# Kernel optimization log

Hardware: AMD Instinct MI355X
Metric: run time of the kernel (lower is better)

Reference implementation:

```python
import jax, jax.numpy as jnp
import numpy as np

T, E, D, F, K, CAP = 4096, 8, 1024, 4096, 2, 1024


def setup_inputs() -> dict:
    key = jax.random.key(0)
    ks = jax.random.split(key, 4)
    x = jax.random.normal(ks[0], (T, D), jnp.float32)
    # top-k routing: mask/weight consistent with a softmax router
    logits = jax.random.normal(ks[1], (T, E), jnp.float32)
    probs = jax.nn.softmax(logits, axis=-1)
    _, topi = jax.lax.top_k(probs, K)  # (T, K)
    route_mask = jnp.zeros((T, E), jnp.bool_).at[jnp.arange(T)[:, None], topi].set(True)
    route_weight = jnp.where(route_mask, probs, 0.0)
    # stacked expert MLP params (E leading axis, as ModuleGroup stacks them)
    w1 = jax.random.normal(ks[2], (E, D, F), jnp.float32) * 0.02
    b1 = jnp.zeros((E, F), jnp.float32)
    w2 = jax.random.normal(ks[3], (E, F, D), jnp.float32) * 0.02
    b2 = jnp.zeros((E, D), jnp.float32)
    return dict(x=x, route_mask=route_mask, route_weight=route_weight,
                w1=w1, b1=b1, w2=w2, b2=b2)


def _build_slots(mask_te, w_te, cap):
    # mask_te: (T,E) bool; w_te: (T,E) float (0 where unrouted)
    Tn, En = mask_te.shape
    m_et = mask_te.T                              # (E,T)
    w_et = jnp.where(m_et, w_te.T, -jnp.inf)      # unrouted -> -inf
    _, idx_top = jax.lax.top_k(w_et, cap)         # (E,C) token ids per slot
    slot = jnp.zeros((En, cap, Tn), w_te.dtype)
    slot = slot.at[jnp.arange(En)[:, None], jnp.arange(cap)[None, :], idx_top].set(1.0)
    slot = slot * m_et[:, None, :].astype(w_te.dtype)  # zero slots from -inf picks
    # NOTE: the original re-orders slots along C (a stable sort); the combine
    # einsum sums over C so the output is invariant to slot order -- skipped.
    return slot


def reference(x, route_mask, route_weight, w1, b1, w2, b2):
    w_te = jnp.where(route_mask, route_weight, 0.0)      # (T,E)
    slot = _build_slots(route_mask, w_te, CAP)           # (E,C,T) one-hot
    # dispatch: 'ect,t...->ec...'
    xs = jnp.einsum('ect,td->ecd', slot, x)              # (E,C,D)
    # expert compute (vmapped MLP over E)
    h = jax.nn.gelu(jnp.einsum('ecd,edf->ecf', xs, w1) + b1[:, None, :])
    out = jnp.einsum('ecf,efd->ecd', h, w2) + b2[:, None, :]
    # combine: 'ecf,ect,te->tf'
    y = jnp.einsum('ecd,ect,te->td', out, slot, w_te)    # (T,D)
    return y
```

## Files before the change

kernel.cpp:

```cpp
#include <hip/hip_runtime.h>
#include <hip/hip_bf16.h>
#include <stdint.h>

#define T_TOK 4096
#define E_EXP 8
#define D_DIM 1024
#define F_DIM 4096
#define K_TOP 2
#define CAPC  1024

typedef __attribute__((ext_vector_type(8))) short short8;
typedef __attribute__((ext_vector_type(4))) float f32x4;
typedef __attribute__((ext_vector_type(4))) unsigned short u16x4;

static __device__ __forceinline__ unsigned short f2bf(float f) {
  union { float f; unsigned u; } v; v.f = f;
  unsigned r = v.u + 0x7fffu + ((v.u >> 16) & 1u);
  return (unsigned short)(r >> 16);
}

static __device__ __forceinline__ void gload_lds16(const void* g, void* l) {
  __builtin_amdgcn_global_load_lds(
      (const __attribute__((address_space(1))) unsigned int*)g,
      (__attribute__((address_space(3))) unsigned int*)l, 16, 0, 0);
}

__global__ void zero_int_kernel(int* p, int n) {
  int i = blockIdx.x * 256 + threadIdx.x;
  if (i < n) p[i] = 0;
}

__global__ __launch_bounds__(1024) void select_kernel(
    const float* __restrict__ rw,
    int* __restrict__ sel_idx,
    int* __restrict__ inv_cnt,
    int* __restrict__ inv_ec,
    float* __restrict__ inv_w)
{
  __shared__ unsigned long long keys[T_TOK];
  const int e = blockIdx.x;
  for (int t = threadIdx.x; t < T_TOK; t += 1024) {
    float w = rw[(size_t)t * E_EXP + e];
    unsigned wb = __float_as_uint(w);
    keys[t] = (w > 0.f)
        ? ((((unsigned long long)wb) << 32) | (unsigned)(T_TOK - 1 - t))
        : 0ull;
  }
  for (int k = 2; k <= T_TOK; k <<= 1) {
    for (int j = k >> 1; j > 0; j >>= 1) {
      __syncthreads();
      for (int i = threadIdx.x; i < T_TOK; i += 1024) {
        int ixj = i ^ j;
        if (ixj > i) {
          unsigned long long a = keys[i], b = keys[ixj];
          bool sw = ((i & k) == 0) ? (a < b) : (a > b);
          if (sw) { keys[i] = b; keys[ixj] = a; }
        }
      }
    }
  }
  __syncthreads();
  for (int c = threadIdx.x; c < CAPC; c += 1024) {
    unsigned long long key = keys[c];
    int t = -1; float w = 0.f;
    if ((key >> 32) != 0ull) {
      t = T_TOK - 1 - (int)(key & 0xffffffffu);
      w = __uint_as_float((unsigned)(key >> 32));
    }
    sel_idx[e * CAPC + c] = t;
    if (t >= 0) {
      int p = atomicAdd(&inv_cnt[t], 1);
      inv_ec[t * K_TOP + p] = e * CAPC + c;
      inv_w[t * K_TOP + p] = w;
    }
  }
}

__global__ void convert_x_kernel(const float* __restrict__ x,
                                 unsigned short* __restrict__ xb, int n4) {
  int i = blockIdx.x * 256 + threadIdx.x;
  if (i >= n4) return;
  f32x4 v = ((const f32x4*)x)[i];
  u16x4 o = { f2bf(v.x), f2bf(v.y), f2bf(v.z), f2bf(v.w) };
  ((u16x4*)xb)[i] = o;
}

__global__ __launch_bounds__(256) void transpose_bf16_kernel(
    const float* __restrict__ in, unsigned short* __restrict__ out,
    int R, int C)
{
  __shared__ unsigned short tile[64][68];
  const int e = blockIdx.z;
  const float* inp = in + (size_t)e * R * C;
  unsigned short* outp = out + (size_t)e * R * C;
  const int c0 = blockIdx.x * 64, r0 = blockIdx.y * 64;
  const int q4 = (threadIdx.x & 15) * 4;
  const int tr = threadIdx.x >> 4;
  for (int rr = tr; rr < 64; rr += 16) {
    f32x4 v = *(const f32x4*)(inp + (size_t)(r0 + rr) * C + c0 + q4);
    tile[rr][q4 + 0] = f2bf(v.x);
    tile[rr][q4 + 1] = f2bf(v.y);
    tile[rr][q4 + 2] = f2bf(v.z);
    tile[rr][q4 + 3] = f2bf(v.w);
  }
  __syncthreads();
  for (int cc = tr; cc < 64; cc += 16) {
    u16x4 o = { tile[q4 + 0][cc], tile[q4 + 1][cc],
                tile[q4 + 2][cc], tile[q4 + 3][cc] };
    *(u16x4*)(outp + (size_t)(c0 + cc) * R + r0 + q4) = o;
  }
}


__global__ __launch_bounds__(256, 3) void gemm1_kernel(
    const unsigned short* __restrict__ xb,
    const int* __restrict__ sel_idx,
    const unsigned short* __restrict__ w1t,
    const float* __restrict__ b1,
    unsigned short* __restrict__ H)
{
  __shared__ __align__(16) unsigned short Asm[128 * 64];
  __shared__ __align__(16) unsigned short Bsm[128 * 64];
  const int e = blockIdx.z;
  const int m0 = blockIdx.y * 128;
  const int n0 = blockIdx.x * 128;
  const int tid = threadIdx.x;
  const int lane = tid & 63, wv = tid >> 6;
  const int wm = (wv >> 1) * 64, wn = (wv & 1) * 64;
  const int lrow = lane & 15, quad = lane >> 4;

  const int rbase = tid >> 3, seg = tid & 7;
  const int cs = seg ^ (rbase & 7);
  const unsigned short* gA[4];
  const unsigned short* gB[4];
  char* lA[4];
  char* lB[4];
  const unsigned short* w1e = w1t + (size_t)e * F_DIM * D_DIM;
#pragma unroll
  for (int it = 0; it < 4; ++it) {
    const int row = rbase + it * 32;
    int t = sel_idx[e * CAPC + m0 + row];
    if (t < 0) t = 0;
    gA[it] = xb + (size_t)t * D_DIM + cs * 8;
    gB[it] = w1e + (size_t)(n0 + row) * D_DIM + cs * 8;
    lA[it] = (char*)Asm + it * 4096 + wv * 1024;
    lB[it] = (char*)Bsm + it * 4096 + wv * 1024;
  }

  f32x4 acc[4][4];
#pragma unroll
  for (int a = 0; a < 4; ++a)
#pragma unroll
    for (int b = 0; b < 4; ++b) acc[a][b] = (f32x4){0.f, 0.f, 0.f, 0.f};

  const int sw = lrow & 7;
  for (int k0 = 0; k0 < D_DIM; k0 += 64) {
#pragma unroll
    for (int it = 0; it < 4; ++it) { gload_lds16(gA[it], lA[it]); gA[it] += 64; }
#pragma unroll
    for (int it = 0; it < 4; ++it) { gload_lds16(gB[it], lB[it]); gB[it] += 64; }
    __syncthreads();
#pragma unroll
    for (int h = 0; h < 2; ++h) {
      short8 af[4], bf[4];
#pragma unroll
      for (int mt = 0; mt < 4; ++mt)
        af[mt] = *(const short8*)(Asm + (wm + mt * 16 + lrow) * 64 +
                                  (((h << 2) + quad) ^ sw) * 8);
#pragma unroll
      for (int nt = 0; nt < 4; ++nt)
        bf[nt] = *(const short8*)(Bsm + (wn + nt * 16 + lrow) * 64 +
                                  (((h << 2) + quad) ^ sw) * 8);
#pragma unroll
      for (int mt = 0; mt < 4; ++mt)
#pragma unroll
        for (int nt = 0; nt < 4; ++nt)
          acc[mt][nt] = __builtin_amdgcn_mfma_f32_16x16x32_bf16(
              af[mt], bf[nt], acc[mt][nt], 0, 0, 0);
    }
    __syncthreads();
  }

  const float* b1e = b1 + e * F_DIM;
#pragma unroll
  for (int nt = 0; nt < 4; ++nt) {
    const int col = n0 + wn + nt * 16 + lrow;
    const float bias = b1e[col];
#pragma unroll
    for (int mt = 0; mt < 4; ++mt) {
      const int rowb = m0 + wm + mt * 16 + quad * 4;
#pragma unroll
      for (int i = 0; i < 4; ++i) {
        float v = acc[mt][nt][i] + bias;
        float u = 0.7978845608028654f * (v + 0.044715f * v * v * v);
        float th = 1.f - 2.f / (1.f + __expf(2.f * u));
        float hv = 0.5f * v * (1.f + th);
        H[((size_t)e * CAPC + rowb + i) * F_DIM + col] = f2bf(hv);
      }
    }
  }
}

__global__ __launch_bounds__(256, 3) void gemm2_kernel(
    const unsigned short* __restrict__ H,
    const unsigned short* __restrict__ w2t,
    const float* __restrict__ b2,
    float* __restrict__ P)
{
  __shared__ __align__(16) unsigned short Asm[128 * 64];
  __shared__ __align__(16) unsigned short Bsm[128 * 64];
  const int e = blockIdx.z & 7;
  const int ks = blockIdx.z >> 3;
  const int m0 = blockIdx.y * 128;
  const int n0 = blockIdx.x * 128;
  const int kbase = ks * (F_DIM / 2);
  const int tid = threadIdx.x;
  const int lane = tid & 63, wv = tid >> 6;
  const int wm = (wv >> 1) * 64, wn = (wv & 1) * 64;
  const int lrow = lane & 15, quad = lane >> 4;

  const int rbase = tid >> 3, seg = tid & 7;
  const int cs = seg ^ (rbase & 7);
  const unsigned short* gA[4];
  const unsigned short* gB[4];
  char* lA[4];
  char* lB[4];
  const unsigned short* He = H + (size_t)e * CAPC * F_DIM;
  const unsigned short* w2e = w2t + (size_t)e * D_DIM * F_DIM;
#pragma unroll
  for (int it = 0; it < 4; ++it) {
    const int row = rbase + it * 32;
    gA[it] = He + (size_t)(m0 + row) * F_DIM + kbase + cs * 8;
    gB[it] = w2e + (size_t)(n0 + row) * F_DIM + kbase + cs * 8;
    lA[it] = (char*)Asm + it * 4096 + wv * 1024;
    lB[it] = (char*)Bsm + it * 4096 + wv * 1024;
  }

  f32x4 acc[4][4];
#pragma unroll
  for (int a = 0; a < 4; ++a)
#pragma unroll
    for (int b = 0; b < 4; ++b) acc[a][b] = (f32x4){0.f, 0.f, 0.f, 0.f};

  const int sw = lrow & 7;
  for (int k0 = 0; k0 < F_DIM / 2; k0 += 64) {
#pragma unroll
    for (int it = 0; it < 4; ++it) { gload_lds16(gA[it], lA[it]); gA[it] += 64; }
#pragma unroll
    for (int it = 0; it < 4; ++it) { gload_lds16(gB[it], lB[it]); gB[it] += 64; }
    __syncthreads();
#pragma unroll
    for (int h = 0; h < 2; ++h) {
      short8 af[4], bf[4];
#pragma unroll
      for (int mt = 0; mt < 4; ++mt)
        af[mt] = *(const short8*)(Asm + (wm + mt * 16 + lrow) * 64 +
                                  (((h << 2) + quad) ^ sw) * 8);
#pragma unroll
      for (int nt = 0; nt < 4; ++nt)
        bf[nt] = *(const short8*)(Bsm + (wn + nt * 16 + lrow) * 64 +
                                  (((h << 2) + quad) ^ sw) * 8);
#pragma unroll
      for (int mt = 0; mt < 4; ++mt)
#pragma unroll
        for (int nt = 0; nt < 4; ++nt)
          acc[mt][nt] = __builtin_amdgcn_mfma_f32_16x16x32_bf16(
              af[mt], bf[nt], acc[mt][nt], 0, 0, 0);
    }
    __syncthreads();
  }

  const float* b2e = b2 + e * D_DIM;
  float* Pk = P + (size_t)ks * E_EXP * CAPC * D_DIM;
#pragma unroll
  for (int nt = 0; nt < 4; ++nt) {
    const int col = n0 + wn + nt * 16 + lrow;
    const float bias = (ks == 0) ? b2e[col] : 0.f;
#pragma unroll
    for (int mt = 0; mt < 4; ++mt) {
      const int rowb = m0 + wm + mt * 16 + quad * 4;
#pragma unroll
      for (int i = 0; i < 4; ++i) {
        Pk[((size_t)e * CAPC + rowb + i) * D_DIM + col] = acc[mt][nt][i] + bias;
      }
    }
  }
}

__global__ __launch_bounds__(256) void combine_kernel(
    const float* __restrict__ P, const int* __restrict__ inv_cnt,
    const int* __restrict__ inv_ec, const float* __restrict__ inv_w,
    float* __restrict__ y)
{
  const int t = blockIdx.x;
  const int cnt = inv_cnt[t];
  f32x4 s = {0.f, 0.f, 0.f, 0.f};
  const int d4 = threadIdx.x;
  const size_t half = (size_t)E_EXP * CAPC * D_DIM;
  for (int p = 0; p < cnt; ++p) {
    const int ec = inv_ec[t * K_TOP + p];
    const float w = inv_w[t * K_TOP + p];
    f32x4 v0 = ((const f32x4*)(P + (size_t)ec * D_DIM))[d4];
    f32x4 v1 = ((const f32x4*)(P + half + (size_t)ec * D_DIM))[d4];
    s += (v0 + v1) * w;
  }
  ((f32x4*)(y + (size_t)t * D_DIM))[d4] = s;
}

extern "C" void kernel_launch(void* const* d_in, const int* in_sizes, int n_in,
                              void* d_out, int out_size, void* d_ws, size_t ws_size,
                              hipStream_t stream) {
  (void)in_sizes; (void)n_in; (void)out_size; (void)ws_size;
  const float* x  = (const float*)d_in[0];
  const float* rw = (const float*)d_in[2];
  const float* w1 = (const float*)d_in[3];
  const float* b1 = (const float*)d_in[4];
  const float* w2 = (const float*)d_in[5];
  const float* b2 = (const float*)d_in[6];
  float* y = (float*)d_out;

  char* ws = (char*)d_ws;
  size_t off = 0;
  auto alloc = [&](size_t bytes) {
    void* p = ws + off;
    off += (bytes + 255) & ~(size_t)255;
    return p;
  };
  unsigned short* xb  = (unsigned short*)alloc((size_t)T_TOK * D_DIM * 2);
  unsigned short* w1t = (unsigned short*)alloc((size_t)E_EXP * F_DIM * D_DIM * 2);
  unsigned short* w2t = (unsigned short*)alloc((size_t)E_EXP * D_DIM * F_DIM * 2);
  unsigned short* H   = (unsigned short*)alloc((size_t)E_EXP * CAPC * F_DIM * 2);
  float* P            = (float*)alloc((size_t)2 * E_EXP * CAPC * D_DIM * 4);
  int* sel_idx        = (int*)alloc((size_t)E_EXP * CAPC * 4);
  int* inv_cnt        = (int*)alloc((size_t)T_TOK * 4);
  int* inv_ec         = (int*)alloc((size_t)T_TOK * K_TOP * 4);
  float* inv_w        = (float*)alloc((size_t)T_TOK * K_TOP * 4);

  zero_int_kernel<<<(T_TOK + 255) / 256, 256, 0, stream>>>(inv_cnt, T_TOK);
  select_kernel<<<E_EXP, 1024, 0, stream>>>(rw, sel_idx, inv_cnt, inv_ec, inv_w);

  convert_x_kernel<<<(T_TOK * D_DIM / 4 + 255) / 256, 256, 0, stream>>>(
      x, xb, T_TOK * D_DIM / 4);
  transpose_bf16_kernel<<<dim3(F_DIM / 64, D_DIM / 64, E_EXP), 256, 0, stream>>>(
      w1, w1t, D_DIM, F_DIM);
  transpose_bf16_kernel<<<dim3(D_DIM / 64, F_DIM / 64, E_EXP), 256, 0, stream>>>(
      w2, w2t, F_DIM, D_DIM);

  gemm1_kernel<<<dim3(F_DIM / 128, CAPC / 128, E_EXP), 256, 0, stream>>>(
      xb, sel_idx, w1t, b1, H);
  gemm2_kernel<<<dim3(D_DIM / 128, CAPC / 128, E_EXP * 2), 256, 0, stream>>>(
      H, w2t, b2, P);

  combine_kernel<<<T_TOK, 256, 0, stream>>>(P, inv_cnt, inv_ec, inv_w, y);
}
```

Measured before the change: 595.6 us.

## Replace bitonic top-k with radix select and remap GEMM blocks for XCD locality

The per-expert selection kernel swaps a full 4096-element bitonic sort of 64-bit keys for an 8-bit-digit radix select that finds the capacity threshold, then compacts winners with atomics and resolves ties with a prefix scan. Separately, both GEMM kernels remap the linear block index so that blocks sharing an expert (and K-split half) land on the same XCD, which is meant to improve L2 reuse of weights and activations. The selection now assigns slots in nondeterministic order and breaks ties by token index rather than by the old ordering. Results should be unaffected because the combine sums over slots.

```diff
diff --git a/kernel.cpp b/kernel.cpp
--- a/kernel.cpp
+++ b/kernel.cpp
@@ -37,41 +37,92 @@
     int* __restrict__ inv_ec,
     float* __restrict__ inv_w)
 {
-  __shared__ unsigned long long keys[T_TOK];
+  __shared__ unsigned keys[T_TOK];
+  __shared__ int hist[256];
+  __shared__ int scan_s[1024];
+  __shared__ int sh_need;
+  __shared__ unsigned sh_prefix;
+  __shared__ int slot_ctr;
   const int e = blockIdx.x;
-  for (int t = threadIdx.x; t < T_TOK; t += 1024) {
+  const int tid = threadIdx.x;
+
+  if (tid < CAPC) sel_idx[e * CAPC + tid] = -1;
+#pragma unroll
+  for (int j = 0; j < 4; ++j) {
+    int t = tid * 4 + j;
     float w = rw[(size_t)t * E_EXP + e];
-    unsigned wb = __float_as_uint(w);
-    keys[t] = (w > 0.f)
-        ? ((((unsigned long long)wb) << 32) | (unsigned)(T_TOK - 1 - t))
-        : 0ull;
-  }
-  for (int k = 2; k <= T_TOK; k <<= 1) {
-    for (int j = k >> 1; j > 0; j >>= 1) {
-      __syncthreads();
-      for (int i = threadIdx.x; i < T_TOK; i += 1024) {
-        int ixj = i ^ j;
-        if (ixj > i) {
-          unsigned long long a = keys[i], b = keys[ixj];
-          bool sw = ((i & k) == 0) ? (a < b) : (a > b);
-          if (sw) { keys[i] = b; keys[ixj] = a; }
-        }
+    keys[t] = (w > 0.f) ? __float_as_uint(w) : 0u;
+  }
+  if (tid == 0) slot_ctr = 0;
+
+  int need = CAPC;
+  unsigned prefix = 0;
+  for (int shift = 24; shift >= 0; shift -= 8) {
+    __syncthreads();
+    if (tid < 256) hist[tid] = 0;
+    __syncthreads();
+#pragma unroll
+    for (int j = 0; j < 4; ++j) {
+      unsigned k = keys[tid * 4 + j];
+      unsigned hi = (shift == 24) ? 0u : (k >> (shift + 8));
+      if (hi == prefix) atomicAdd(&hist[(k >> shift) & 255u], 1);
+    }
+    __syncthreads();
+    if (tid == 0) {
+      int cum = 0, b = 0;
+      for (b = 255; b >= 0; --b) {
+        cum += hist[b];
+        if (cum >= need) break;
       }
-    }
-  }
+      if (b < 0) b = 0;
+      sh_need = need - (cum - hist[b]);
+      sh_prefix = (prefix << 8) | (unsigned)b;
+    }
+    __syncthreads();
+    need = sh_need;
+    prefix = sh_prefix;
+  }
+  const unsigned thr = prefix;
   __syncthreads();
-  for (int c = threadIdx.x; c < CAPC; c += 1024) {
-    unsigned long long key = keys[c];
-    int t = -1; float w = 0.f;
-    if ((key >> 32) != 0ull) {
-      t = T_TOK - 1 - (int)(key & 0xffffffffu);
-      w = __uint_as_float((unsigned)(key >> 32));
-    }
-    sel_idx[e * CAPC + c] = t;
-    if (t >= 0) {
+
+  int eqflag[4], myeq = 0;
+#pragma unroll
+  for (int j = 0; j < 4; ++j) {
+    const int t = tid * 4 + j;
+    const unsigned k = keys[t];
+    if (k > thr) {
+      int s = atomicAdd(&slot_ctr, 1);
+      sel_idx[e * CAPC + s] = t;
       int p = atomicAdd(&inv_cnt[t], 1);
-      inv_ec[t * K_TOP + p] = e * CAPC + c;
-      inv_w[t * K_TOP + p] = w;
+      inv_ec[t * K_TOP + p] = e * CAPC + s;
+      inv_w[t * K_TOP + p] = __uint_as_float(k);
+    }
+    eqflag[j] = (thr > 0u && k == thr) ? 1 : 0;
+    myeq += eqflag[j];
+  }
+  scan_s[tid] = myeq;
+  __syncthreads();
+  for (int d = 1; d < 1024; d <<= 1) {
+    int v = scan_s[tid];
+    int add = (tid >= d) ? scan_s[tid - d] : 0;
+    __syncthreads();
+    scan_s[tid] = v + add;
+    __syncthreads();
+  }
+  int r = scan_s[tid] - myeq;
+  const int base = CAPC - need;
+#pragma unroll
+  for (int j = 0; j < 4; ++j) {
+    if (eqflag[j]) {
+      if (r < need) {
+        const int t = tid * 4 + j;
+        const int s = base + r;
+        sel_idx[e * CAPC + s] = t;
+        int p = atomicAdd(&inv_cnt[t], 1);
+        inv_ec[t * K_TOP + p] = e * CAPC + s;
+        inv_w[t * K_TOP + p] = __uint_as_float(thr);
+      }
+      ++r;
     }
   }
 }
@@ -119,11 +170,16 @@
     const float* __restrict__ b1,
     unsigned short* __restrict__ H)
 {
+  const int lin = blockIdx.x + 32 * (blockIdx.y + 8 * blockIdx.z);
+  const int e = lin & 7;
+  const int slot = lin >> 3;
+  const int xb_ = slot >> 3;
+  const int yb_ = slot & 7;
+  const int m0 = yb_ * 128;
+  const int n0 = xb_ * 128;
+
   __shared__ __align__(16) unsigned short Asm[128 * 64];
   __shared__ __align__(16) unsigned short Bsm[128 * 64];
-  const int e = blockIdx.z;
-  const int m0 = blockIdx.y * 128;
-  const int n0 = blockIdx.x * 128;
   const int tid = threadIdx.x;
   const int lane = tid & 63, wv = tid >> 6;
   const int wm = (wv >> 1) * 64, wn = (wv & 1) * 64;
@@ -207,13 +263,21 @@
     const float* __restrict__ b2,
     float* __restrict__ P)
 {
+  const int lin = blockIdx.x + 8 * (blockIdx.y + 8 * blockIdx.z);
+  const int xcd = lin & 7;
+  const int slot = lin >> 3;
+  const int g = xcd * 2 + (slot >> 6);
+  const int e = g & 7;
+  const int ks = g >> 3;
+  const int tile = slot & 63;
+  const int xb_ = tile >> 3;
+  const int yb_ = tile & 7;
+  const int m0 = yb_ * 128;
+  const int n0 = xb_ * 128;
+  const int kbase = ks * (F_DIM / 2);
+
   __shared__ __align__(16) unsigned short Asm[128 * 64];
   __shared__ __align__(16) unsigned short Bsm[128 * 64];
-  const int e = blockIdx.z & 7;
-  const int ks = blockIdx.z >> 3;
-  const int m0 = blockIdx.y * 128;
-  const int n0 = blockIdx.x * 128;
-  const int kbase = ks * (F_DIM / 2);
   const int tid = threadIdx.x;
   const int lane = tid & 63, wv = tid >> 6;
   const int wm = (wv >> 1) * 64, wn = (wv & 1) * 64;
```

Result: slower. 612.3 us (+2.8%).
